# Kernel optimization log

Hardware: AMD Instinct MI355X
Metric: run time of the kernel (lower is better)

Reference implementation:

```python
import jax, jax.numpy as jnp
import numpy as np

N, S, F, D = 4096, 128, 128, 256  # batch, memory slots, feat_dim, dim_h_o
EPS = 1e-8  # torch CosineSimilarity eps


def _xavier(key, shape):
    fan_out, fan_in = shape
    std = float(np.sqrt(2.0 / (fan_in + fan_out)))
    return jax.random.normal(key, shape, dtype=jnp.float32) * std


def setup_inputs() -> dict:
    key = jax.random.key(0)
    ks = jax.random.split(key, 10)
    return {
        "h_o_prev": jax.random.normal(ks[0], (N, D), dtype=jnp.float32),
        "C": jax.random.normal(ks[1], (N, S, F), dtype=jnp.float32),
        "Wk": _xavier(ks[2], (F, D)), "bk": jnp.zeros((F,), jnp.float32),
        "Wb": _xavier(ks[3], (1, D)), "bb": jnp.zeros((1,), jnp.float32),
        "We": _xavier(ks[4], (F, D)), "be": jnp.zeros((F,), jnp.float32),
        "Wv": _xavier(ks[5], (F, D)), "bv": jnp.zeros((F,), jnp.float32),
        "Wih": _xavier(ks[6], (3 * D, F)), "Whh": _xavier(ks[7], (3 * D, D)),
        "bih": jnp.zeros((3 * D,), jnp.float32), "bhh": jnp.zeros((3 * D,), jnp.float32),
    }


def reference(h_o_prev, C, Wk, bk, Wb, bb, We, be, Wv, bv, Wih, Whh, bih, bhh):
    # --- Attention (content addressing) ---
    k = h_o_prev @ Wk.T + bk                              # [N, F]
    beta_pre = h_o_prev @ Wb.T + bb                       # [N, 1]
    # clamp-split softplus trick in source == softplus(x) + 1
    beta = jax.nn.softplus(beta_pre) + 1.0                # [N, 1]
    C_norm = jnp.maximum(jnp.linalg.norm(C, axis=2), EPS)           # [N, S]
    k_norm = jnp.maximum(jnp.linalg.norm(k, axis=1, keepdims=True), EPS)  # [N, 1]
    s = jnp.einsum("nsf,nf->ns", C, k) / (C_norm * k_norm)          # cosine sim [N, S]
    w = jax.nn.softmax(s * beta, axis=1)                  # [N, S]
    # --- Read memory ---
    r = jnp.einsum("ns,nsf->nf", w, C)                    # [N, F]
    # --- GRU cell update (torch GRUCell semantics) ---
    gi = r @ Wih.T + bih                                  # [N, 3D]
    gh = h_o_prev @ Whh.T + bhh                           # [N, 3D]
    i_r, i_z, i_n = jnp.split(gi, 3, axis=1)
    h_r, h_z, h_n = jnp.split(gh, 3, axis=1)
    rg = jax.nn.sigmoid(i_r + h_r)
    z = jax.nn.sigmoid(i_z + h_z)
    n = jnp.tanh(i_n + rg * h_n)
    h_o = (1.0 - z) * n + z * h_o_prev                    # [N, D]
    # --- Write memory (erase + add, outer products) ---
    e = jax.nn.sigmoid(h_o @ We.T + be)                   # [N, F]
    v = h_o @ Wv.T + bv                                   # [N, F]
    w2 = w[:, :, None]                                    # [N, S, 1]
    C_new = C * (1.0 - w2 * e[:, None, :]) + w2 * v[:, None, :]
    return h_o, C_new, k, r
```

## Files before the change

kernel.cpp:

```cpp
#include <hip/hip_runtime.h>
#include <hip/hip_bf16.h>
#include <cstddef>
#include <cstdint>

constexpr int Nn = 4096;
constexpr int Ss = 128;
constexpr int Ff = 128;
constexpr int Dd = 256;
constexpr float EPSV = 1e-8f;

constexpr size_t HO_OFF = 0;
constexpr size_t C_OFF  = (size_t)Nn * Dd;
constexpr size_t K_OFF  = C_OFF + (size_t)Nn * Ss * Ff;
constexpr size_t R_OFF  = K_OFF + (size_t)Nn * Ff;

typedef __attribute__((ext_vector_type(4))) float f4v;
typedef __attribute__((ext_vector_type(8))) short bh8;
typedef __attribute__((ext_vector_type(4))) short bh4;

constexpr int WK_O  = 0;
constexpr int WHH_O = 32768;
constexpr int WIH_O = 229376;
constexpr int WEV_O = 327680;
constexpr int W_TOT = 393216;

#define WAITVM(N) asm volatile("s_waitcnt vmcnt(" #N ")" ::: "memory")

__device__ __forceinline__ float sigmf(float x) { return 1.0f / (1.0f + __expf(-x)); }

__device__ __forceinline__ short f2bf(float x) {
    __hip_bfloat16 h = __float2bfloat16(x);
    return *reinterpret_cast<short*>(&h);
}

__device__ __forceinline__ void gll16(const float* g, float* l) {
    __builtin_amdgcn_global_load_lds(
        (const __attribute__((address_space(1))) void*)g,
        (__attribute__((address_space(3))) void*)l,
        16, 0, 0);
}

__device__ __forceinline__ int swzH(int row, int kb) { return row * 512 + (kb ^ ((row & 7) << 4)); }
__device__ __forceinline__ int swzR(int row, int kb) { return row * 256 + (kb ^ ((row & 7) << 4)); }

__device__ __forceinline__ f4v mfma16(bh8 a, bh8 b, f4v c) {
    return __builtin_amdgcn_mfma_f32_16x16x32_bf16(a, b, c, 0, 0, 0);
}

__global__ __launch_bounds__(256) void prep_weights(
    const float* __restrict__ Wk, const float* __restrict__ Whh,
    const float* __restrict__ Wih, const float* __restrict__ We,
    const float* __restrict__ Wv, short* __restrict__ out)
{
    int id = blockIdx.x * 256 + threadIdx.x;
    float v;
    if      (id < WHH_O) v = Wk[id - WK_O];
    else if (id < WIH_O) v = Whh[id - WHH_O];
    else if (id < WEV_O) v = Wih[id - WIH_O];
    else if (id < WEV_O + 32768) v = We[id - WEV_O];
    else v = Wv[id - WEV_O - 32768];
    out[id] = f2bf(v);
}

__global__ __launch_bounds__(512, 2) void mega_kernel(
    const float* __restrict__ C, const float* __restrict__ h_prev,
    const short* __restrict__ WB,
    const float* __restrict__ Wb, const float* __restrict__ bb,
    const float* __restrict__ bk, const float* __restrict__ bhh,
    const float* __restrict__ bih, const float* __restrict__ be,
    const float* __restrict__ bv,
    float* __restrict__ ho, float* __restrict__ Cnew,
    float* __restrict__ kout, float* __restrict__ rout)
{
    __shared__ float sH[8][256];
    __shared__ __align__(16) short sHb[16 * 256];
    __shared__ __align__(16) short sRb[16 * 128];
    __shared__ float sK[8][128];
    __shared__ float sSc[8][128];
    __shared__ float sEV[8][256];
    __shared__ __align__(16) float sStage[8][1024];

    const int t  = threadIdx.x;
    const int l  = t & 63;
    const int wv = t >> 6;
    const int nb = blockIdx.x * 8;
    char* hb = (char*)sHb;
    char* rb = (char*)sRb;

    const short* WkB  = WB + WK_O;
    const short* WhhB = WB + WHH_O;
    const short* WihB = WB + WIH_O;
    const short* WevB = WB + WEV_O;

    {
        const int f = t * 4, row = f >> 8, col = f & 255;
        float4 hv = *(const float4*)(h_prev + (size_t)(nb + row) * Dd + col);
        *(float4*)&sH[row][col] = hv;
        bh4 hb4 = { f2bf(hv.x), f2bf(hv.y), f2bf(hv.z), f2bf(hv.w) };
        *(bh4*)(hb + swzH(row, col * 2)) = hb4;
        *(int64_t*)(hb + 4096 + t * 8) = 0;
        *(int*)(rb + 2048 + t * 4) = 0;
    }
    __syncthreads();

    {
        const int fr = l & 15, kq = l >> 4, rbase = kq * 4;
        const int colg = wv * 16 + fr;
        f4v acc = {0.f, 0.f, 0.f, 0.f};
#pragma unroll
        for (int kc = 0; kc < 8; ++kc) {
            bh8 a = *(const bh8*)(hb + swzH(fr, kc * 64 + kq * 16));
            bh8 b = *(const bh8*)(WkB + (size_t)colg * 256 + kc * 32 + kq * 8);
            acc = mfma16(a, b, acc);
        }
        if (rbase < 8) {
            const float bs = bk[colg];
#pragma unroll
            for (int rg = 0; rg < 4; ++rg) {
                float x = acc[rg] + bs;
                sK[rbase + rg][colg] = x;
                kout[(size_t)(nb + rbase + rg) * Ff + colg] = x;
            }
        }
    }
    __syncthreads();

    float invL_r = 0.0f;
    {
        const int half = l >> 5, fl = l & 31, f4 = fl * 4;
        const float* Cn = C + (size_t)(nb + wv) * (Ss * Ff);

        float kv0 = sK[wv][l], kv1 = sK[wv][64 + l];
        float ks = kv0 * kv0 + kv1 * kv1;
#pragma unroll
        for (int o = 32; o > 0; o >>= 1) ks += __shfl_xor(ks, o);
        const float knorm = fmaxf(sqrtf(ks), EPSV);

        float4 hv = *(const float4*)&sH[wv][l * 4];
        float4 wb4 = *(const float4*)(Wb + l * 4);
        float bp = hv.x * wb4.x + hv.y * wb4.y + hv.z * wb4.z + hv.w * wb4.w;
#pragma unroll
        for (int o = 32; o > 0; o >>= 1) bp += __shfl_xor(bp, o);
        bp += bb[0];
        const float beta = ((bp > 20.0f) ? bp : log1pf(__expf(bp))) + 1.0f;

        const float4 kreg = *(const float4*)&sK[wv][f4];
        float lsum = 0.0f;
        f4v racc = {0.f, 0.f, 0.f, 0.f};
        float* stg = &sStage[wv][0];

        WAITVM(0);
#pragma unroll
        for (int k = 0; k < 4; ++k)
            gll16(Cn + k * 256 + l * 4, stg + k * 256);

#pragma unroll 4
        for (int k = 0; k < 64; ++k) {
            WAITVM(3);
            const f4v c4 = *(const f4v*)(stg + (k & 3) * 256 + l * 4);
            float d = c4.x * kreg.x + c4.y * kreg.y + c4.z * kreg.z + c4.w * kreg.w;
            float q = c4.x * c4.x + c4.y * c4.y + c4.z * c4.z + c4.w * c4.w;
            if (k < 60)
                gll16(Cn + (k + 4) * 256 + l * 4, stg + (k & 3) * 256);
#pragma unroll
            for (int o = 16; o > 0; o >>= 1) {
                d += __shfl_xor(d, o);
                q += __shfl_xor(q, o);
            }
            const int s = k * 2 + half;
            const float cn = fmaxf(sqrtf(q), EPSV);
            const float x = d / (cn * knorm) * beta;
            const float p = __expf(x - beta);
            if (fl == 0) sSc[wv][s] = p;
            lsum += p;
            racc += p * c4;
        }
        const float L = lsum + __shfl_xor(lsum, 32);
        f4v r2;
        r2.x = __shfl_xor(racc.x, 32); r2.y = __shfl_xor(racc.y, 32);
        r2.z = __shfl_xor(racc.z, 32); r2.w = __shfl_xor(racc.w, 32);
        const float iL = 1.0f / L;
        f4v r4 = (racc + r2) * iL;
        if (half == 0) {
            *(f4v*)(rout + (size_t)(nb + wv) * Ff + f4) = r4;
            bh4 rb4 = { f2bf(r4.x), f2bf(r4.y), f2bf(r4.z), f2bf(r4.w) };
            *(bh4*)(rb + swzR(wv, f4 * 2)) = rb4;
        }
        invL_r = iL;
    }
    __syncthreads();

    {
        const int fr = l & 15, kq = l >> 4, rbase = kq * 4;
        f4v aG[6], aI[6];
#pragma unroll
        for (int i = 0; i < 6; ++i) {
            const int colg = i * 128 + wv * 16 + fr;
            f4v g = {0.f, 0.f, 0.f, 0.f}, ii = {0.f, 0.f, 0.f, 0.f};
#pragma unroll
            for (int kc = 0; kc < 8; ++kc) {
                bh8 a = *(const bh8*)(hb + swzH(fr, kc * 64 + kq * 16));
                bh8 b = *(const bh8*)(WhhB + (size_t)colg * 256 + kc * 32 + kq * 8);
                g = mfma16(a, b, g);
            }
#pragma unroll
            for (int kc = 0; kc < 4; ++kc) {
                bh8 a = *(const bh8*)(rb + swzR(fr, kc * 64 + kq * 16));
                bh8 b = *(const bh8*)(WihB + (size_t)colg * 128 + kc * 32 + kq * 8);
                ii = mfma16(a, b, ii);
            }
            aG[i] = g; aI[i] = ii;
        }

        float hoReg[2][4];
        if (rbase < 8) {
#pragma unroll
            for (int dp = 0; dp < 2; ++dp) {
                const int d = dp * 128 + wv * 16 + fr;
                const float br  = bhh[d] + bih[d];
                const float bz  = bhh[256 + d] + bih[256 + d];
                const float bhn = bhh[512 + d];
                const float bin = bih[512 + d];
#pragma unroll
                for (int rg = 0; rg < 4; ++rg) {
                    const float rgt = sigmf(aG[dp][rg] + aI[dp][rg] + br);
                    const float z   = sigmf(aG[2 + dp][rg] + aI[2 + dp][rg] + bz);
                    const float nn  = tanhf(aI[4 + dp][rg] + bin + rgt * (aG[4 + dp][rg] + bhn));
                    const float hp  = sH[rbase + rg][d];
                    hoReg[dp][rg] = (1.0f - z) * nn + z * hp;
                }
            }
        }
        __syncthreads();
        if (rbase < 8) {
#pragma unroll
            for (int dp = 0; dp < 2; ++dp) {
                const int d = dp * 128 + wv * 16 + fr;
#pragma unroll
                for (int rg = 0; rg < 4; ++rg) {
                    const int row = rbase + rg;
                    const float o = hoReg[dp][rg];
                    ho[(size_t)(nb + row) * Dd + d] = o;
                    *(short*)(hb + row * 512 + ((d * 2) ^ ((row & 7) << 4))) = f2bf(o);
                }
            }
        }
    }
    __syncthreads();

    {
        const int fr = l & 15, kq = l >> 4, rbase = kq * 4;
#pragma unroll
        for (int i = 0; i < 2; ++i) {
            const int colg = i * 128 + wv * 16 + fr;
            f4v acc = {0.f, 0.f, 0.f, 0.f};
#pragma unroll
            for (int kc = 0; kc < 8; ++kc) {
                bh8 a = *(const bh8*)(hb + swzH(fr, kc * 64 + kq * 16));
                bh8 b = *(const bh8*)(WevB + (size_t)colg * 256 + kc * 32 + kq * 8);
                acc = mfma16(a, b, acc);
            }
            if (rbase < 8) {
                const float bs = (colg < 128) ? be[colg] : bv[colg - 128];
#pragma unroll
                for (int rg = 0; rg < 4; ++rg) {
                    float x = acc[rg] + bs;
                    if (colg < 128) x = sigmf(x);
                    sEV[rbase + rg][colg] = x;
                }
            }
        }
    }
    __syncthreads();

    {
        const int half = l >> 5, fl = l & 31, f4 = fl * 4;
        const float* Cn = C    + (size_t)(nb + wv) * (Ss * Ff);
        float*       Co = Cnew + (size_t)(nb + wv) * (Ss * Ff);
        const f4v e4 = *(const f4v*)&sEV[wv][f4];
        const f4v v4 = *(const f4v*)&sEV[wv][128 + f4];
        const float iL = invL_r;
        float* stg = &sStage[wv][0];

        WAITVM(0);
#pragma unroll 1
        for (int b = 0; b < 16; ++b) {
#pragma unroll
            for (int j = 0; j < 4; ++j)
                gll16(Cn + (b * 4 + j) * 256 + l * 4, stg + j * 256);
            WAITVM(0);
#pragma unroll
            for (int j = 0; j < 4; ++j) {
                const int s = b * 8 + j * 2 + half;
                const f4v c4 = *(const f4v*)(stg + j * 256 + l * 4);
                const float wsc = sSc[wv][s] * iL;
                f4v o = c4 * (1.0f - wsc * e4) + wsc * v4;
                __builtin_nontemporal_store(o, (f4v*)(Co + (size_t)s * Ff + f4));
            }
        }
    }
}

extern "C" void kernel_launch(void* const* d_in, const int* in_sizes, int n_in,
                              void* d_out, int out_size, void* d_ws, size_t ws_size,
                              hipStream_t stream)
{
    const float* h_prev = (const float*)d_in[0];
    const float* C      = (const float*)d_in[1];
    const float* Wk     = (const float*)d_in[2];
    const float* bk     = (const float*)d_in[3];
    const float* Wb     = (const float*)d_in[4];
    const float* bb     = (const float*)d_in[5];
    const float* We     = (const float*)d_in[6];
    const float* be     = (const float*)d_in[7];
    const float* Wv     = (const float*)d_in[8];
    const float* bv     = (const float*)d_in[9];
    const float* Wih    = (const float*)d_in[10];
    const float* Whh    = (const float*)d_in[11];
    const float* bih    = (const float*)d_in[12];
    const float* bhh    = (const float*)d_in[13];

    float* out  = (float*)d_out;
    float* ho   = out + HO_OFF;
    float* Cnew = out + C_OFF;
    float* kbuf = out + K_OFF;
    float* rbuf = out + R_OFF;

    short* wsB = (short*)d_ws;

    prep_weights<<<W_TOT / 256, 256, 0, stream>>>(Wk, Whh, Wih, We, Wv, wsB);

    mega_kernel<<<Nn / 8, 512, 0, stream>>>(
        C, h_prev, wsB, Wb, bb, bk, bhh, bih, be, bv,
        ho, Cnew, kbuf, rbuf);
}
```

Measured before the change: 197.3 us.

## Split fused mega kernel into four stage kernels with workspace intermediates

Replaces the single fused kernel with four launches: k/beta/gh projection, per-row attention over C with 256 threads per batch row, GRU plus erase/add projections, and a flat grid-stride elementwise memory update. The aim is more parallelism and occupancy in the C-streaming phases, which were limited by one wave per row and large LDS staging. In exchange, C is read twice from global memory instead of once from global and once more within the same block, and gh, w and e/v take extra round trips through workspace. Three more kernel launches are also added.

```diff
diff --git a/kernel.cpp b/kernel.cpp
--- a/kernel.cpp
+++ b/kernel.cpp
@@ -24,20 +24,11 @@
 constexpr int WEV_O = 327680;
 constexpr int W_TOT = 393216;
 
-#define WAITVM(N) asm volatile("s_waitcnt vmcnt(" #N ")" ::: "memory")
-
 __device__ __forceinline__ float sigmf(float x) { return 1.0f / (1.0f + __expf(-x)); }
 
 __device__ __forceinline__ short f2bf(float x) {
     __hip_bfloat16 h = __float2bfloat16(x);
     return *reinterpret_cast<short*>(&h);
-}
-
-__device__ __forceinline__ void gll16(const float* g, float* l) {
-    __builtin_amdgcn_global_load_lds(
-        (const __attribute__((address_space(1))) void*)g,
-        (__attribute__((address_space(3))) void*)l,
-        16, 0, 0);
 }
 
 __device__ __forceinline__ int swzH(int row, int kb) { return row * 512 + (kb ^ ((row & 7) << 4)); }
@@ -62,23 +53,165 @@
     out[id] = f2bf(v);
 }
 
-__global__ __launch_bounds__(512, 2) void mega_kernel(
-    const float* __restrict__ C, const float* __restrict__ h_prev,
-    const short* __restrict__ WB,
+__global__ __launch_bounds__(512, 2) void k1_pre(
+    const float* __restrict__ h_prev, const short* __restrict__ WB,
     const float* __restrict__ Wb, const float* __restrict__ bb,
-    const float* __restrict__ bk, const float* __restrict__ bhh,
-    const float* __restrict__ bih, const float* __restrict__ be,
-    const float* __restrict__ bv,
-    float* __restrict__ ho, float* __restrict__ Cnew,
-    float* __restrict__ kout, float* __restrict__ rout)
+    const float* __restrict__ bk,
+    float* __restrict__ kout, float* __restrict__ beta_out,
+    float* __restrict__ gh_out)
+{
+    __shared__ float sH[8][256];
+    __shared__ __align__(16) short sHb[16 * 256];
+
+    const int t  = threadIdx.x;
+    const int l  = t & 63;
+    const int wv = t >> 6;
+    const int nb = blockIdx.x * 8;
+    char* hb = (char*)sHb;
+
+    const short* WkB  = WB + WK_O;
+    const short* WhhB = WB + WHH_O;
+
+    {
+        const int f = t * 4, row = f >> 8, col = f & 255;
+        float4 hv = *(const float4*)(h_prev + (size_t)(nb + row) * Dd + col);
+        *(float4*)&sH[row][col] = hv;
+        bh4 hb4 = { f2bf(hv.x), f2bf(hv.y), f2bf(hv.z), f2bf(hv.w) };
+        *(bh4*)(hb + swzH(row, col * 2)) = hb4;
+        *(int64_t*)(hb + 4096 + t * 8) = 0;
+    }
+    __syncthreads();
+
+    const int fr = l & 15, kq = l >> 4, rbase = kq * 4;
+
+    {
+        const int colg = wv * 16 + fr;
+        f4v acc = {0.f, 0.f, 0.f, 0.f};
+#pragma unroll
+        for (int kc = 0; kc < 8; ++kc) {
+            bh8 a = *(const bh8*)(hb + swzH(fr, kc * 64 + kq * 16));
+            bh8 b = *(const bh8*)(WkB + (size_t)colg * 256 + kc * 32 + kq * 8);
+            acc = mfma16(a, b, acc);
+        }
+        if (rbase < 8) {
+            const float bs = bk[colg];
+#pragma unroll
+            for (int rg = 0; rg < 4; ++rg)
+                kout[(size_t)(nb + rbase + rg) * Ff + colg] = acc[rg] + bs;
+        }
+    }
+
+    {
+        float4 hv = *(const float4*)&sH[wv][l * 4];
+        float4 wb4 = *(const float4*)(Wb + l * 4);
+        float bp = hv.x * wb4.x + hv.y * wb4.y + hv.z * wb4.z + hv.w * wb4.w;
+#pragma unroll
+        for (int o = 32; o > 0; o >>= 1) bp += __shfl_xor(bp, o);
+        if (l == 0) {
+            bp += bb[0];
+            beta_out[nb + wv] = ((bp > 20.0f) ? bp : log1pf(__expf(bp))) + 1.0f;
+        }
+    }
+
+    {
+#pragma unroll
+        for (int i = 0; i < 6; ++i) {
+            const int colg = i * 128 + wv * 16 + fr;
+            f4v g = {0.f, 0.f, 0.f, 0.f};
+#pragma unroll
+            for (int kc = 0; kc < 8; ++kc) {
+                bh8 a = *(const bh8*)(hb + swzH(fr, kc * 64 + kq * 16));
+                bh8 b = *(const bh8*)(WhhB + (size_t)colg * 256 + kc * 32 + kq * 8);
+                g = mfma16(a, b, g);
+            }
+            if (rbase < 8) {
+#pragma unroll
+                for (int rg = 0; rg < 4; ++rg)
+                    gh_out[(size_t)(nb + rbase + rg) * 768 + colg] = g[rg];
+            }
+        }
+    }
+}
+
+__global__ __launch_bounds__(256, 6) void k2_attn(
+    const float* __restrict__ C, const float* __restrict__ kin,
+    const float* __restrict__ beta_in,
+    float* __restrict__ w_out, float* __restrict__ r_out)
+{
+    __shared__ float sk[128];
+    __shared__ float sSc[128];
+    __shared__ float sred[4];
+    __shared__ float sr4[4][128];
+
+    const int n    = blockIdx.x;
+    const int t    = threadIdx.x;
+    const int lane = t & 63;
+    const int wid  = t >> 6;
+    const float* Cn = C + (size_t)n * (Ss * Ff);
+
+    if (t < 128) sk[t] = kin[(size_t)n * Ff + t];
+    __syncthreads();
+
+    float kv0 = sk[lane], kv1 = sk[64 + lane];
+    float ks = kv0 * kv0 + kv1 * kv1;
+#pragma unroll
+    for (int o = 32; o > 0; o >>= 1) ks += __shfl_xor(ks, o);
+    const float knorm = fmaxf(sqrtf(ks), EPSV);
+    const float beta  = beta_in[n];
+
+    const int sub = lane >> 5, fl = lane & 31, f4 = fl * 4;
+    const float4 kreg = *(const float4*)&sk[f4];
+    float lsum = 0.0f;
+    f4v racc = {0.f, 0.f, 0.f, 0.f};
+
+#pragma unroll 8
+    for (int it = 0; it < 16; ++it) {
+        const int s = wid * 32 + it * 2 + sub;
+        const f4v c4 = *(const f4v*)(Cn + (size_t)s * Ff + f4);
+        float d = c4.x * kreg.x + c4.y * kreg.y + c4.z * kreg.z + c4.w * kreg.w;
+        float q = c4.x * c4.x + c4.y * c4.y + c4.z * c4.z + c4.w * c4.w;
+#pragma unroll
+        for (int o = 16; o > 0; o >>= 1) {
+            d += __shfl_xor(d, o);
+            q += __shfl_xor(q, o);
+        }
+        const float cn = fmaxf(sqrtf(q), EPSV);
+        const float x = d / (cn * knorm) * beta;
+        const float p = __expf(x - beta);
+        if (fl == 0) sSc[s] = p;
+        lsum += p;
+        racc += p * c4;
+    }
+    lsum += __shfl_xor(lsum, 32);
+    racc.x += __shfl_xor(racc.x, 32);
+    racc.y += __shfl_xor(racc.y, 32);
+    racc.z += __shfl_xor(racc.z, 32);
+    racc.w += __shfl_xor(racc.w, 32);
+    if (lane == 0) sred[wid] = lsum;
+    if (sub == 0) *(f4v*)&sr4[wid][f4] = racc;
+    __syncthreads();
+
+    const float iL = 1.0f / (sred[0] + sred[1] + sred[2] + sred[3]);
+    if (t < 128) w_out[(size_t)n * Ss + t] = sSc[t] * iL;
+    if (t < 32) {
+        f4v rr = *(f4v*)&sr4[0][t * 4];
+#pragma unroll
+        for (int g = 1; g < 4; ++g) rr += *(f4v*)&sr4[g][t * 4];
+        rr *= iL;
+        *(f4v*)(r_out + (size_t)n * Ff + t * 4) = rr;
+    }
+}
+
+__global__ __launch_bounds__(512, 2) void k3_post(
+    const float* __restrict__ h_prev, const short* __restrict__ WB,
+    const float* __restrict__ gh_in, const float* __restrict__ rin,
+    const float* __restrict__ bhh, const float* __restrict__ bih,
+    const float* __restrict__ be, const float* __restrict__ bv,
+    float* __restrict__ ho, float* __restrict__ ev_out)
 {
     __shared__ float sH[8][256];
     __shared__ __align__(16) short sHb[16 * 256];
     __shared__ __align__(16) short sRb[16 * 128];
-    __shared__ float sK[8][128];
-    __shared__ float sSc[8][128];
-    __shared__ float sEV[8][256];
-    __shared__ __align__(16) float sStage[8][1024];
 
     const int t  = threadIdx.x;
     const int l  = t & 63;
@@ -87,133 +220,52 @@
     char* hb = (char*)sHb;
     char* rb = (char*)sRb;
 
-    const short* WkB  = WB + WK_O;
-    const short* WhhB = WB + WHH_O;
     const short* WihB = WB + WIH_O;
     const short* WevB = WB + WEV_O;
 
     {
-        const int f = t * 4, row = f >> 8, col = f & 255;
-        float4 hv = *(const float4*)(h_prev + (size_t)(nb + row) * Dd + col);
-        *(float4*)&sH[row][col] = hv;
-        bh4 hb4 = { f2bf(hv.x), f2bf(hv.y), f2bf(hv.z), f2bf(hv.w) };
-        *(bh4*)(hb + swzH(row, col * 2)) = hb4;
-        *(int64_t*)(hb + 4096 + t * 8) = 0;
-        *(int*)(rb + 2048 + t * 4) = 0;
+        const int row = t >> 6, col = (t & 63) * 4;
+        *(float4*)&sH[row][col] = *(const float4*)(h_prev + (size_t)(nb + row) * Dd + col);
+        if (t < 256) {
+            const int rr = t >> 5, rc = (t & 31) * 4;
+            float4 rv = *(const float4*)(rin + (size_t)(nb + rr) * Ff + rc);
+            bh4 rb4 = { f2bf(rv.x), f2bf(rv.y), f2bf(rv.z), f2bf(rv.w) };
+            *(bh4*)(rb + swzR(rr, rc * 2)) = rb4;
+        } else {
+            const int tt = t - 256;
+            *(int64_t*)(rb + 2048 + tt * 8) = 0;
+            *(int4*)(hb + 4096 + tt * 16) = int4{0, 0, 0, 0};
+        }
     }
     __syncthreads();
 
-    {
-        const int fr = l & 15, kq = l >> 4, rbase = kq * 4;
-        const int colg = wv * 16 + fr;
-        f4v acc = {0.f, 0.f, 0.f, 0.f};
-#pragma unroll
-        for (int kc = 0; kc < 8; ++kc) {
-            bh8 a = *(const bh8*)(hb + swzH(fr, kc * 64 + kq * 16));
-            bh8 b = *(const bh8*)(WkB + (size_t)colg * 256 + kc * 32 + kq * 8);
-            acc = mfma16(a, b, acc);
-        }
-        if (rbase < 8) {
-            const float bs = bk[colg];
-#pragma unroll
-            for (int rg = 0; rg < 4; ++rg) {
-                float x = acc[rg] + bs;
-                sK[rbase + rg][colg] = x;
-                kout[(size_t)(nb + rbase + rg) * Ff + colg] = x;
-            }
-        }
-    }
-    __syncthreads();
-
-    float invL_r = 0.0f;
-    {
-        const int half = l >> 5, fl = l & 31, f4 = fl * 4;
-        const float* Cn = C + (size_t)(nb + wv) * (Ss * Ff);
-
-        float kv0 = sK[wv][l], kv1 = sK[wv][64 + l];
-        float ks = kv0 * kv0 + kv1 * kv1;
-#pragma unroll
-        for (int o = 32; o > 0; o >>= 1) ks += __shfl_xor(ks, o);
-        const float knorm = fmaxf(sqrtf(ks), EPSV);
-
-        float4 hv = *(const float4*)&sH[wv][l * 4];
-        float4 wb4 = *(const float4*)(Wb + l * 4);
-        float bp = hv.x * wb4.x + hv.y * wb4.y + hv.z * wb4.z + hv.w * wb4.w;
-#pragma unroll
-        for (int o = 32; o > 0; o >>= 1) bp += __shfl_xor(bp, o);
-        bp += bb[0];
-        const float beta = ((bp > 20.0f) ? bp : log1pf(__expf(bp))) + 1.0f;
-
-        const float4 kreg = *(const float4*)&sK[wv][f4];
-        float lsum = 0.0f;
-        f4v racc = {0.f, 0.f, 0.f, 0.f};
-        float* stg = &sStage[wv][0];
-
-        WAITVM(0);
-#pragma unroll
-        for (int k = 0; k < 4; ++k)
-            gll16(Cn + k * 256 + l * 4, stg + k * 256);
-
-#pragma unroll 4
-        for (int k = 0; k < 64; ++k) {
-            WAITVM(3);
-            const f4v c4 = *(const f4v*)(stg + (k & 3) * 256 + l * 4);
-            float d = c4.x * kreg.x + c4.y * kreg.y + c4.z * kreg.z + c4.w * kreg.w;
-            float q = c4.x * c4.x + c4.y * c4.y + c4.z * c4.z + c4.w * c4.w;
-            if (k < 60)
-                gll16(Cn + (k + 4) * 256 + l * 4, stg + (k & 3) * 256);
-#pragma unroll
-            for (int o = 16; o > 0; o >>= 1) {
-                d += __shfl_xor(d, o);
-                q += __shfl_xor(q, o);
-            }
-            const int s = k * 2 + half;
-            const float cn = fmaxf(sqrtf(q), EPSV);
-            const float x = d / (cn * knorm) * beta;
-            const float p = __expf(x - beta);
-            if (fl == 0) sSc[wv][s] = p;
-            lsum += p;
-            racc += p * c4;
-        }
-        const float L = lsum + __shfl_xor(lsum, 32);
-        f4v r2;
-        r2.x = __shfl_xor(racc.x, 32); r2.y = __shfl_xor(racc.y, 32);
-        r2.z = __shfl_xor(racc.z, 32); r2.w = __shfl_xor(racc.w, 32);
-        const float iL = 1.0f / L;
-        f4v r4 = (racc + r2) * iL;
-        if (half == 0) {
-            *(f4v*)(rout + (size_t)(nb + wv) * Ff + f4) = r4;
-            bh4 rb4 = { f2bf(r4.x), f2bf(r4.y), f2bf(r4.z), f2bf(r4.w) };
-            *(bh4*)(rb + swzR(wv, f4 * 2)) = rb4;
-        }
-        invL_r = iL;
-    }
-    __syncthreads();
-
-    {
-        const int fr = l & 15, kq = l >> 4, rbase = kq * 4;
-        f4v aG[6], aI[6];
+    const int fr = l & 15, kq = l >> 4, rbase = kq * 4;
+
+    {
+        f4v aI[6];
 #pragma unroll
         for (int i = 0; i < 6; ++i) {
             const int colg = i * 128 + wv * 16 + fr;
-            f4v g = {0.f, 0.f, 0.f, 0.f}, ii = {0.f, 0.f, 0.f, 0.f};
-#pragma unroll
-            for (int kc = 0; kc < 8; ++kc) {
-                bh8 a = *(const bh8*)(hb + swzH(fr, kc * 64 + kq * 16));
-                bh8 b = *(const bh8*)(WhhB + (size_t)colg * 256 + kc * 32 + kq * 8);
-                g = mfma16(a, b, g);
-            }
+            f4v ii = {0.f, 0.f, 0.f, 0.f};
 #pragma unroll
             for (int kc = 0; kc < 4; ++kc) {
                 bh8 a = *(const bh8*)(rb + swzR(fr, kc * 64 + kq * 16));
                 bh8 b = *(const bh8*)(WihB + (size_t)colg * 128 + kc * 32 + kq * 8);
                 ii = mfma16(a, b, ii);
             }
-            aG[i] = g; aI[i] = ii;
+            aI[i] = ii;
         }
 
         float hoReg[2][4];
         if (rbase < 8) {
+            float aG[6][4];
+#pragma unroll
+            for (int i = 0; i < 6; ++i) {
+                const int colg = i * 128 + wv * 16 + fr;
+#pragma unroll
+                for (int rg = 0; rg < 4; ++rg)
+                    aG[i][rg] = gh_in[(size_t)(nb + rbase + rg) * 768 + colg];
+            }
 #pragma unroll
             for (int dp = 0; dp < 2; ++dp) {
                 const int d = dp * 128 + wv * 16 + fr;
@@ -249,7 +301,6 @@
     __syncthreads();
 
     {
-        const int fr = l & 15, kq = l >> 4, rbase = kq * 4;
 #pragma unroll
         for (int i = 0; i < 2; ++i) {
             const int colg = i * 128 + wv * 16 + fr;
@@ -266,37 +317,40 @@
                 for (int rg = 0; rg < 4; ++rg) {
                     float x = acc[rg] + bs;
                     if (colg < 128) x = sigmf(x);
-                    sEV[rbase + rg][colg] = x;
+                    ev_out[(size_t)(nb + rbase + rg) * 256 + colg] = x;
                 }
             }
         }
     }
-    __syncthreads();
-
-    {
-        const int half = l >> 5, fl = l & 31, f4 = fl * 4;
-        const float* Cn = C    + (size_t)(nb + wv) * (Ss * Ff);
-        float*       Co = Cnew + (size_t)(nb + wv) * (Ss * Ff);
-        const f4v e4 = *(const f4v*)&sEV[wv][f4];
-        const f4v v4 = *(const f4v*)&sEV[wv][128 + f4];
-        const float iL = invL_r;
-        float* stg = &sStage[wv][0];
-
-        WAITVM(0);
+}
+
+__global__ __launch_bounds__(256, 4) void k4_update(
+    const float* __restrict__ C, const float* __restrict__ w,
+    const float* __restrict__ ev, float* __restrict__ Cnew)
+{
+    const size_t stride = (size_t)2048 * 256;
+    const size_t i0 = (size_t)blockIdx.x * 256 + threadIdx.x;
 #pragma unroll 1
-        for (int b = 0; b < 16; ++b) {
-#pragma unroll
-            for (int j = 0; j < 4; ++j)
-                gll16(Cn + (b * 4 + j) * 256 + l * 4, stg + j * 256);
-            WAITVM(0);
-#pragma unroll
-            for (int j = 0; j < 4; ++j) {
-                const int s = b * 8 + j * 2 + half;
-                const f4v c4 = *(const f4v*)(stg + j * 256 + l * 4);
-                const float wsc = sSc[wv][s] * iL;
-                f4v o = c4 * (1.0f - wsc * e4) + wsc * v4;
-                __builtin_nontemporal_store(o, (f4v*)(Co + (size_t)s * Ff + f4));
-            }
+    for (int rep = 0; rep < 32; rep += 4) {
+        f4v c[4], e4[4], v4[4];
+        float wsc[4];
+#pragma unroll
+        for (int j = 0; j < 4; ++j) {
+            const size_t i = i0 + (size_t)(rep + j) * stride;
+            const int n = (int)(i >> 12);
+            const int rem = (int)(i & 4095);
+            const int s = rem >> 5;
+            const int f4 = (rem & 31) * 4;
+            c[j]   = *(const f4v*)(C + i * 4);
+            wsc[j] = w[(size_t)n * Ss + s];
+            e4[j]  = *(const f4v*)(ev + (size_t)n * 256 + f4);
+            v4[j]  = *(const f4v*)(ev + (size_t)n * 256 + 128 + f4);
+        }
+#pragma unroll
+        for (int j = 0; j < 4; ++j) {
+            const size_t i = i0 + (size_t)(rep + j) * stride;
+            f4v o = c[j] * (1.0f - wsc[j] * e4[j]) + wsc[j] * v4[j];
+            __builtin_nontemporal_store(o, (f4v*)(Cnew + i * 4));
         }
     }
 }
@@ -327,10 +381,21 @@
     float* rbuf = out + R_OFF;
 
     short* wsB = (short*)d_ws;
+    float* wsF     = (float*)(wsB + W_TOT);
+    float* ws_gh   = wsF;
+    float* ws_beta = ws_gh + (size_t)Nn * 768;
+    float* ws_w    = ws_beta + Nn;
+    float* ws_ev   = ws_w + (size_t)Nn * Ss;
 
     prep_weights<<<W_TOT / 256, 256, 0, stream>>>(Wk, Whh, Wih, We, Wv, wsB);
 
-    mega_kernel<<<Nn / 8, 512, 0, stream>>>(
-        C, h_prev, wsB, Wb, bb, bk, bhh, bih, be, bv,
-        ho, Cnew, kbuf, rbuf);
-}
+    k1_pre<<<Nn / 8, 512, 0, stream>>>(h_prev, wsB, Wb, bb, bk,
+                                       kbuf, ws_beta, ws_gh);
+
+    k2_attn<<<Nn, 256, 0, stream>>>(C, kbuf, ws_beta, ws_w, rbuf);
+
+    k3_post<<<Nn / 8, 512, 0, stream>>>(h_prev, wsB, ws_gh, rbuf,
+                                        bhh, bih, be, bv, ho, ws_ev);
+
+    k4_update<<<2048, 256, 0, stream>>>(C, ws_w, ws_ev, Cnew);
+}
```

After: 224.8 us. 13.9% more time.

## Drop LDS staging of C, load directly to registers, raise occupancy

Applied to the files above, without the earlier changes.

Removes the per-wave 32KB LDS staging buffer and its global_load_lds pipeline, replacing it with direct vectorized global loads of C in both the attention pass and the write pass. The GRU MFMA accumulation is restructured to handle one half of the output columns at a time, cutting live accumulator registers from twelve to six vectors. Launch bounds are raised from 2 to 6 blocks per CU. Together these aim to raise occupancy so that memory latency is hidden by more resident waves instead of explicit prefetch, at the cost of relying on the compiler and hardware for latency hiding and possibly register spills under the tighter bound.

```diff
diff --git a/kernel.cpp b/kernel.cpp
--- a/kernel.cpp
+++ b/kernel.cpp
@@ -24,20 +24,11 @@
 constexpr int WEV_O = 327680;
 constexpr int W_TOT = 393216;
 
-#define WAITVM(N) asm volatile("s_waitcnt vmcnt(" #N ")" ::: "memory")
-
 __device__ __forceinline__ float sigmf(float x) { return 1.0f / (1.0f + __expf(-x)); }
 
 __device__ __forceinline__ short f2bf(float x) {
     __hip_bfloat16 h = __float2bfloat16(x);
     return *reinterpret_cast<short*>(&h);
-}
-
-__device__ __forceinline__ void gll16(const float* g, float* l) {
-    __builtin_amdgcn_global_load_lds(
-        (const __attribute__((address_space(1))) void*)g,
-        (__attribute__((address_space(3))) void*)l,
-        16, 0, 0);
 }
 
 __device__ __forceinline__ int swzH(int row, int kb) { return row * 512 + (kb ^ ((row & 7) << 4)); }
@@ -62,7 +53,7 @@
     out[id] = f2bf(v);
 }
 
-__global__ __launch_bounds__(512, 2) void mega_kernel(
+__global__ __launch_bounds__(512, 6) void mega_kernel(
     const float* __restrict__ C, const float* __restrict__ h_prev,
     const short* __restrict__ WB,
     const float* __restrict__ Wb, const float* __restrict__ bb,
@@ -78,7 +69,6 @@
     __shared__ float sK[8][128];
     __shared__ float sSc[8][128];
     __shared__ float sEV[8][256];
-    __shared__ __align__(16) float sStage[8][1024];
 
     const int t  = threadIdx.x;
     const int l  = t & 63;
@@ -147,27 +137,18 @@
         const float4 kreg = *(const float4*)&sK[wv][f4];
         float lsum = 0.0f;
         f4v racc = {0.f, 0.f, 0.f, 0.f};
-        float* stg = &sStage[wv][0];
-
-        WAITVM(0);
-#pragma unroll
-        for (int k = 0; k < 4; ++k)
-            gll16(Cn + k * 256 + l * 4, stg + k * 256);
 
 #pragma unroll 4
         for (int k = 0; k < 64; ++k) {
-            WAITVM(3);
-            const f4v c4 = *(const f4v*)(stg + (k & 3) * 256 + l * 4);
+            const int s = k * 2 + half;
+            const f4v c4 = *(const f4v*)(Cn + (size_t)s * Ff + f4);
             float d = c4.x * kreg.x + c4.y * kreg.y + c4.z * kreg.z + c4.w * kreg.w;
             float q = c4.x * c4.x + c4.y * c4.y + c4.z * c4.z + c4.w * c4.w;
-            if (k < 60)
-                gll16(Cn + (k + 4) * 256 + l * 4, stg + (k & 3) * 256);
 #pragma unroll
             for (int o = 16; o > 0; o >>= 1) {
                 d += __shfl_xor(d, o);
                 q += __shfl_xor(q, o);
             }
-            const int s = k * 2 + half;
             const float cn = fmaxf(sqrtf(q), EPSV);
             const float x = d / (cn * knorm) * beta;
             const float p = __expf(x - beta);
@@ -192,30 +173,29 @@
 
     {
         const int fr = l & 15, kq = l >> 4, rbase = kq * 4;
-        f4v aG[6], aI[6];
-#pragma unroll
-        for (int i = 0; i < 6; ++i) {
-            const int colg = i * 128 + wv * 16 + fr;
-            f4v g = {0.f, 0.f, 0.f, 0.f}, ii = {0.f, 0.f, 0.f, 0.f};
-#pragma unroll
-            for (int kc = 0; kc < 8; ++kc) {
-                bh8 a = *(const bh8*)(hb + swzH(fr, kc * 64 + kq * 16));
-                bh8 b = *(const bh8*)(WhhB + (size_t)colg * 256 + kc * 32 + kq * 8);
-                g = mfma16(a, b, g);
-            }
-#pragma unroll
-            for (int kc = 0; kc < 4; ++kc) {
-                bh8 a = *(const bh8*)(rb + swzR(fr, kc * 64 + kq * 16));
-                bh8 b = *(const bh8*)(WihB + (size_t)colg * 128 + kc * 32 + kq * 8);
-                ii = mfma16(a, b, ii);
-            }
-            aG[i] = g; aI[i] = ii;
-        }
-
         float hoReg[2][4];
-        if (rbase < 8) {
-#pragma unroll
-            for (int dp = 0; dp < 2; ++dp) {
+#pragma unroll
+        for (int dp = 0; dp < 2; ++dp) {
+            f4v aG[3], aI[3];
+#pragma unroll
+            for (int gi = 0; gi < 3; ++gi) {
+                const int colg = (gi * 2 + dp) * 128 + wv * 16 + fr;
+                f4v g = {0.f, 0.f, 0.f, 0.f}, ii = {0.f, 0.f, 0.f, 0.f};
+#pragma unroll
+                for (int kc = 0; kc < 8; ++kc) {
+                    bh8 a = *(const bh8*)(hb + swzH(fr, kc * 64 + kq * 16));
+                    bh8 b = *(const bh8*)(WhhB + (size_t)colg * 256 + kc * 32 + kq * 8);
+                    g = mfma16(a, b, g);
+                }
+#pragma unroll
+                for (int kc = 0; kc < 4; ++kc) {
+                    bh8 a = *(const bh8*)(rb + swzR(fr, kc * 64 + kq * 16));
+                    bh8 b = *(const bh8*)(WihB + (size_t)colg * 128 + kc * 32 + kq * 8);
+                    ii = mfma16(a, b, ii);
+                }
+                aG[gi] = g; aI[gi] = ii;
+            }
+            if (rbase < 8) {
                 const int d = dp * 128 + wv * 16 + fr;
                 const float br  = bhh[d] + bih[d];
                 const float bz  = bhh[256 + d] + bih[256 + d];
@@ -223,9 +203,9 @@
                 const float bin = bih[512 + d];
 #pragma unroll
                 for (int rg = 0; rg < 4; ++rg) {
-                    const float rgt = sigmf(aG[dp][rg] + aI[dp][rg] + br);
-                    const float z   = sigmf(aG[2 + dp][rg] + aI[2 + dp][rg] + bz);
-                    const float nn  = tanhf(aI[4 + dp][rg] + bin + rgt * (aG[4 + dp][rg] + bhn));
+                    const float rgt = sigmf(aG[0][rg] + aI[0][rg] + br);
+                    const float z   = sigmf(aG[1][rg] + aI[1][rg] + bz);
+                    const float nn  = tanhf(aI[2][rg] + bin + rgt * (aG[2][rg] + bhn));
                     const float hp  = sH[rbase + rg][d];
                     hoReg[dp][rg] = (1.0f - z) * nn + z * hp;
                 }
@@ -280,23 +260,14 @@
         const f4v e4 = *(const f4v*)&sEV[wv][f4];
         const f4v v4 = *(const f4v*)&sEV[wv][128 + f4];
         const float iL = invL_r;
-        float* stg = &sStage[wv][0];
-
-        WAITVM(0);
-#pragma unroll 1
-        for (int b = 0; b < 16; ++b) {
-#pragma unroll
-            for (int j = 0; j < 4; ++j)
-                gll16(Cn + (b * 4 + j) * 256 + l * 4, stg + j * 256);
-            WAITVM(0);
-#pragma unroll
-            for (int j = 0; j < 4; ++j) {
-                const int s = b * 8 + j * 2 + half;
-                const f4v c4 = *(const f4v*)(stg + j * 256 + l * 4);
-                const float wsc = sSc[wv][s] * iL;
-                f4v o = c4 * (1.0f - wsc * e4) + wsc * v4;
-                __builtin_nontemporal_store(o, (f4v*)(Co + (size_t)s * Ff + f4));
-            }
+
+#pragma unroll 4
+        for (int k = 0; k < 64; ++k) {
+            const int s = k * 2 + half;
+            const f4v c4 = *(const f4v*)(Cn + (size_t)s * Ff + f4);
+            const float wsc = sSc[wv][s] * iL;
+            f4v o = c4 * (1.0f - wsc * e4) + wsc * v4;
+            __builtin_nontemporal_store(o, (f4v*)(Co + (size_t)s * Ff + f4));
         }
     }
 }
```

Result: slower. 221.1 us (+12.1%).
